# Performance work log

Hardware: AMD Instinct MI355X
Metric: run time of the kernel (lower is better)

## Reference

```python
import jax, jax.numpy as jnp
import numpy as np

NB = 4
QN = -(2 ** (NB - 1))   # -8
QP = 2 ** (NB - 1) - 1  # 7
EPS = 1e-5


def _grad_scale(x, g):
    # forward: x, backward: grad * g (LSQ gradient scaling)
    return x * g + jax.lax.stop_gradient(x - x * g)


def _round_pass(x):
    # round with straight-through estimator
    return x + jax.lax.stop_gradient(jnp.round(x) - x)


def _lsq(v, alpha, qn, qp):
    # LSQ fake quantize-dequantize with learnable step size alpha
    g = 1.0 / np.sqrt(v.size * qp)
    a = _grad_scale(alpha, g)
    return _round_pass(jnp.clip(v / a, qn, qp)) * a


def _bn(x, g, b, m, v):
    # eval-mode BatchNorm2d over channel dim of NCHW
    s = (g * jax.lax.rsqrt(v + EPS))[None, :, None, None]
    return (x - m[None, :, None, None]) * s + b[None, :, None, None]


def _conv(x, w, stride, pad, groups):
    return jax.lax.conv_general_dilated(
        x, w, (stride, stride), pad,
        dimension_numbers=('NCHW', 'OIHW', 'NCHW'),
        feature_group_count=groups)


def setup_inputs() -> dict:
    key = jax.random.key(0)
    ks = jax.random.split(key, 4)
    inp, oup, hid = 96, 96, 576
    B, H, W = 32, 28, 28
    d = {}
    d['x'] = jax.random.normal(ks[0], (B, inp, H, W), jnp.float32)
    d['w1'] = jax.random.normal(ks[1], (hid, inp, 1, 1), jnp.float32) * 0.1
    d['w2'] = jax.random.normal(ks[2], (hid, 1, 3, 3), jnp.float32) * 0.1
    d['w3'] = jax.random.normal(ks[3], (oup, hid, 1, 1), jnp.float32) * 0.1
    for i, c in zip((1, 2, 3), (hid, hid, oup)):
        d[f'aw{i}'] = jnp.full((1,), 0.05, jnp.float32)  # weight step size
        d[f'ax{i}'] = jnp.full((1,), 0.5, jnp.float32)   # activation step size
        d[f'g{i}'] = jnp.ones((c,), jnp.float32)
        d[f'b{i}'] = jnp.zeros((c,), jnp.float32)
        d[f'm{i}'] = jnp.zeros((c,), jnp.float32)
        d[f'v{i}'] = jnp.ones((c,), jnp.float32)
    return d


def reference(x, w1, w2, w3, aw1, ax1, g1, b1, m1, v1,
              aw2, ax2, g2, b2, m2, v2, aw3, ax3, g3, b3, m3, v3):
    hid = w1.shape[0]
    # 1x1 expand conv (LSQ on activation and weight)
    h = _conv(_lsq(x, ax1, QN, QP), _lsq(w1, aw1, QN, QP), 1, [(0, 0), (0, 0)], 1)
    h = jnp.clip(_bn(h, g1, b1, m1, v1), 0.0, 6.0)
    # 3x3 depthwise conv, stride 1
    h = _conv(_lsq(h, ax2, QN, QP), _lsq(w2, aw2, QN, QP), 1, [(1, 1), (1, 1)], hid)
    h = jnp.clip(_bn(h, g2, b2, m2, v2), 0.0, 6.0)
    # 1x1 project conv
    h = _conv(_lsq(h, ax3, QN, QP), _lsq(w3, aw3, QN, QP), 1, [(0, 0), (0, 0)], 1)
    h = _bn(h, g3, b3, m3, v3)
    # identity residual (stride==1 and inp==oup)
    return x + h
```

## Files before the change

### kernel.cpp

```cpp
#include <hip/hip_runtime.h>

#define EPSF 1e-5f
#define MAGICF 12582912.0f
#define MLO 0x4B3FFFF8
#define MHI 0x4B400007

typedef int    int4v   __attribute__((ext_vector_type(4)));
typedef float  float4v __attribute__((ext_vector_type(4)));

#define W1P_OFF  0
#define W3P_OFF  55296
#define W2T_OFF  110592
#define S1B1_OFF 119808
#define S2B2_OFF 124416
#define S3B3_OFF 129024

#define F1S 296
#define H2S 304

__device__ __forceinline__ float lsq_q(float v, float a) {
    float t = v / a;
    t = fminf(fmaxf(t, -8.0f), 7.0f);
    return rintf(t);
}

__device__ __forceinline__ long q8pack_w(const float* w, int base, const int* idx, float a) {
    unsigned long long v = 0;
    #pragma unroll
    for (int j = 0; j < 8; ++j) {
        int q = (int)lsq_q(w[base + idx[j]], a);
        v |= (unsigned long long)(q & 255) << (8 * j);
    }
    return (long)v;
}

__global__ __launch_bounds__(128)
void prep_w(const float* __restrict__ w1, const float* __restrict__ w2,
            const float* __restrict__ w3,
            const float* aw1, const float* ax1, const float* ax2,
            const float* aw2, const float* ax3, const float* aw3,
            const float* __restrict__ g1, const float* __restrict__ b1,
            const float* __restrict__ m1, const float* __restrict__ v1,
            const float* __restrict__ g2, const float* __restrict__ b2,
            const float* __restrict__ m2, const float* __restrict__ v2,
            const float* __restrict__ g3, const float* __restrict__ b3,
            const float* __restrict__ m3, const float* __restrict__ v3,
            long* __restrict__ w1p, long* __restrict__ w3p,
            int* __restrict__ w2t,
            float* __restrict__ s1b1, float* __restrict__ s2b2,
            float* __restrict__ s3b3) {
    int id = blockIdx.x * 128 + threadIdx.x;
    const int lin[8] = {0, 1, 2, 3, 4, 5, 6, 7};
    const int prm[8] = {0, 2, 4, 6, 1, 3, 5, 7};
    if (id < 6912) {
        int l = id & 63, t = id >> 6;
        int kc = t % 3, ct = t / 3;
        int co = ct * 16 + (l & 15);
        int ci0 = kc * 32 + (l >> 4) * 8;
        w1p[id] = q8pack_w(w1, co * 96 + ci0, lin, aw1[0]);
    } else if (id < 13824) {
        int i = id - 6912;
        int l = i & 63, t = i >> 6;
        int kc = t % 18, ct = t / 18;
        int co = ct * 16 + (l & 15);
        int ci0 = kc * 32 + (l >> 4) * 8;
        w3p[i] = q8pack_w(w3, co * 576 + ci0, prm, aw3[0]);
    } else if (id < 14400) {
        int ch = id - 13824;
        int q[9];
        #pragma unroll
        for (int tp = 0; tp < 9; ++tp)
            q[tp] = (int)lsq_q(w2[ch * 9 + tp], aw2[0]) & 255;
        w2t[ch * 4 + 0] = q[0] | (q[1] << 8) | (q[2] << 16) | (q[3] << 24);
        w2t[ch * 4 + 1] = q[4] | (q[5] << 8) | (q[6] << 16) | (q[7] << 24);
        w2t[ch * 4 + 2] = q[8];
        w2t[ch * 4 + 3] = 0;
    } else if (id < 14976) {
        int c = id - 14400;
        float s = g1[c] / sqrtf(v1[c] + EPSF);
        float A = aw1[0] * ax1[0];
        float inv = 1.0f / ax2[0];
        s1b1[c] = A * s * inv;
        s1b1[576 + c] = (b1[c] - m1[c] * s) * inv;
    } else if (id < 15552) {
        int c = id - 14976;
        float s = g2[c] / sqrtf(v2[c] + EPSF);
        float A = ax2[0] * aw2[0];
        float inv = 1.0f / ax3[0];
        s2b2[c] = A * s * inv;
        s2b2[576 + c] = (b2[c] - m2[c] * s) * inv;
    } else if (id < 15648) {
        int c = id - 15552;
        float s = g3[c] / sqrtf(v3[c] + EPSF);
        float A = ax3[0] * aw3[0];
        s3b3[c] = A * s;
        s3b3[96 + c] = b3[c] - m3[c] * s;
    }
}

__global__ __launch_bounds__(512, 4)
void fused_k(const float* __restrict__ x, const long* __restrict__ w1p,
             const int* __restrict__ w2tg, const long* __restrict__ w3p,
             const float* __restrict__ ax1,
             const float* __restrict__ s1b1g, const float* __restrict__ s2b2g,
             const float* __restrict__ s3b3g, float* __restrict__ out) {
    __shared__ __align__(16) char smem[74176];
    signed char* h1 = (signed char*)smem;
    float*       l1 = (float*)(smem + 35520);
    signed char* h2 = (signed char*)(smem + 40128);
    float*       l2 = (float*)(smem + 59584);
    float*       l3 = (float*)(smem + 64192);
    int4v*      l2t = (int4v*)(smem + 64960);
    long*    wstage = (long*)h2;
    long*       w3s = (long*)smem;

    const int tid = threadIdx.x;
    const int w = tid >> 6, l = tid & 63;
    const int quad = l >> 4, c16 = l & 15;
    const int qh = quad >> 1, ql = quad & 1;
    const int b = blockIdx.x;
    const int r0 = blockIdx.y * 2;
    const bool awork = (w < 7);

    {
        const int lp = w * 16 + c16;
        const int row = lp / 28, col = lp - (lp / 28) * 28;
        const int img_row = r0 - 1 + row;
        const bool valid = awork && ((unsigned)img_row < 28u);
        const int p = min(max(img_row, 0), 27) * 28 + col;
        const float inv1 = 1.0f / ax1[0];

        float xv[3][8];
        if (awork) {
            #pragma unroll
            for (int kc = 0; kc < 3; ++kc) {
                const float* xs = x + (b * 96 + kc * 32 + quad * 8) * 784 + p;
                #pragma unroll
                for (int j = 0; j < 8; ++j) xv[kc][j] = xs[j * 784];
            }
        }

        for (int i = tid; i < 35520 / 16; i += 512)
            ((int4v*)h1)[i] = (int4v){0, 0, 0, 0};
        if (tid < 288) {
            ((int4v*)l1)[tid] = ((const int4v*)s1b1g)[tid];
            ((int4v*)l2)[tid] = ((const int4v*)s2b2g)[tid];
        }
        if (tid < 48) ((int4v*)l3)[tid] = ((const int4v*)s3b3g)[tid];
        for (int i = tid; i < 576; i += 512) l2t[i] = ((const int4v*)w2tg)[i];
        for (int i = tid; i < 1152; i += 512) wstage[i] = w1p[i];
        __syncthreads();

        long bfr[3];
        if (awork) {
            #pragma unroll
            for (int kc = 0; kc < 3; ++kc) {
                unsigned long long v = 0;
                #pragma unroll
                for (int j = 0; j < 8; ++j) {
                    int qi = __float_as_int(fmaf(xv[kc][j], inv1, MAGICF));
                    qi = min(max(qi, MLO), MHI);
                    v |= (unsigned long long)(qi & 255) << (8 * j);
                }
                bfr[kc] = (long)v;
            }
        }
        const int pos_h = row * 30 + col + 1;

        for (int c = 0; c < 6; ++c) {
            if (!awork) {
                if (c < 5) {
                    const long* src = w1p + (c + 1) * 1152;
                    long stg[18];
                    #pragma unroll
                    for (int k = 0; k < 18; ++k) stg[k] = src[l + k * 64];
                    long* dst = wstage + ((c + 1) & 1) * 1152;
                    #pragma unroll
                    for (int k = 0; k < 18; ++k) dst[l + k * 64] = stg[k];
                }
            } else {
                const long* cur = wstage + (c & 1) * 1152;
                #pragma unroll 3
                for (int ctl = 0; ctl < 6; ++ctl) {
                    const int ct = c * 6 + ctl;
                    int4v acc; acc[0] = 0; acc[1] = 0; acc[2] = 0; acc[3] = 0;
                    #pragma unroll
                    for (int kc = 0; kc < 3; ++kc)
                        acc = __builtin_amdgcn_mfma_i32_16x16x32_i8(
                            cur[(ctl * 3 + kc) * 64 + l], bfr[kc], acc, 0, 0, 0);
                    const int co0 = ct * 16 + quad * 4;
                    float4v S = *(const float4v*)(l1 + co0);
                    float4v B = *(const float4v*)(l1 + 576 + co0);
                    int pk = 0;
                    #pragma unroll
                    for (int r2 = 0; r2 < 4; ++r2) {
                        float t = fmaf((float)acc[r2], S[r2], B[r2]);
                        t = __builtin_amdgcn_fmed3f(t, 0.0f, 7.0f);
                        pk |= (__float_as_int(t + MAGICF) & 15) << (4 * r2);
                    }
                    if (valid)
                        *(unsigned short*)(h1 + pos_h * F1S + (co0 >> 1))
                            = (unsigned short)pk;
                }
            }
            __syncthreads();
        }
    }

    {
        const bool vald = ((c16 >> 3) == ql);
        const int mh = c16 & 7;
        const int jj = (mh >> 1) | ((mh & 1) << 2);
        const unsigned shla = 8u * (jj & 3);
        const unsigned mlo = (jj < 4) ? 0xFFFFFFFFu : 0u;
        const unsigned mhi = ~mlo;
        const unsigned vm  = vald ? 0xFFu : 0u;
        const unsigned vm4 = (vald && qh == 0) ? 0xFFu : 0u;
        const unsigned sh0 = qh * 8u;
        const unsigned sh1 = 16u + qh * 8u;

        #pragma unroll 2
        for (int t = w; t < 144; t += 8) {
            const int pt = t / 36, ct = t - (t / 36) * 36;
            const int pos = pt * 16 + c16;
            const int posc = min(pos, 55);
            const int row_in = posc / 28, col = posc - (posc / 28) * 28;
            const int choff = ct * 8 + ql * 4;
            const int4v tw = l2t[ct * 16 + c16];
            int4v acc; acc[0] = 0; acc[1] = 0; acc[2] = 0; acc[3] = 0;
            #pragma unroll
            for (int kc = 0; kc < 5; ++kc) {
                unsigned bb;
                if      (kc == 0) bb = ((unsigned)tw[0] >> sh0) & vm;
                else if (kc == 1) bb = ((unsigned)tw[0] >> sh1) & vm;
                else if (kc == 2) bb = ((unsigned)tw[1] >> sh0) & vm;
                else if (kc == 3) bb = ((unsigned)tw[1] >> sh1) & vm;
                else              bb = ((unsigned)tw[2]) & vm4;
                const unsigned pl = bb << shla;
                const long afrag = (long)(((unsigned long long)(pl & mhi) << 32)
                                          | (pl & mlo));
                const int tap = min(kc * 2 + qh, 8);
                const int dh = tap / 3 - 1, dc = tap - (tap / 3) * 3 - 1;
                const int pos_h = (row_in + 1 + dh) * 30 + (col + 1 + dc);
                const unsigned v = *(const unsigned*)(h1 + pos_h * F1S + choff);
                const unsigned lo = v & 0x0F0F0F0Fu;
                const unsigned hi = (v >> 4) & 0x0F0F0F0Fu;
                acc = __builtin_amdgcn_mfma_i32_16x16x32_i8(
                    afrag, (long)(((unsigned long long)hi << 32) | lo), acc, 0, 0, 0);
            }
            if (pos < 56) {
                const int c0 = ct * 16 + quad * 4;
                float4v S = *(const float4v*)(l2 + c0);
                float4v B = *(const float4v*)(l2 + 576 + c0);
                int pk = 0;
                #pragma unroll
                for (int r2 = 0; r2 < 4; ++r2) {
                    float tt = fmaf((float)acc[r2], S[r2], B[r2]);
                    tt = __builtin_amdgcn_fmed3f(tt, 0.0f, 7.0f);
                    pk |= (__float_as_int(tt + MAGICF) & 15) << (4 * r2);
                }
                *(unsigned short*)(h2 + pos * H2S + (c0 >> 1)) = (unsigned short)pk;
            }
        }
    }

    {
        long stg[5];
        auto c3_issue = [&](int ck) {
            #pragma unroll
            for (int k = 0; k < 5; ++k) {
                const int e = tid + k * 512;
                if (e < 2304) {
                    const int ct2 = e / 384, rem = e - ct2 * 384;
                    stg[k] = w3p[ct2 * 1152 + ck * 384 + rem];
                }
            }
        };
        auto c3_write = [&](int buf) {
            #pragma unroll
            for (int k = 0; k < 5; ++k) {
                const int e = tid + k * 512;
                if (e < 2304) w3s[buf * 2304 + e] = stg[k];
            }
        };

        int4v accs[3];
        #pragma unroll
        for (int tt = 0; tt < 3; ++tt) {
            accs[tt][0] = 0; accs[tt][1] = 0; accs[tt][2] = 0; accs[tt][3] = 0;
        }
        auto c3_compute = [&](int ck, int buf) {
            #pragma unroll
            for (int tt = 0; tt < 3; ++tt) {
                const int t = w + tt * 8;
                const int nt = t / 6, ct = t - (t / 6) * 6;
                const signed char* arow = h2 + (nt * 16 + c16) * H2S + quad * 4;
                #pragma unroll
                for (int kcl = 0; kcl < 6; ++kcl) {
                    const int kc = ck * 6 + kcl;
                    const unsigned va = *(const unsigned*)(arow + kc * 16);
                    const unsigned lo = va & 0x0F0F0F0Fu;
                    const unsigned hi = (va >> 4) & 0x0F0F0F0Fu;
                    accs[tt] = __builtin_amdgcn_mfma_i32_16x16x32_i8(
                        (long)(((unsigned long long)hi << 32) | lo),
                        w3s[buf * 2304 + (ct * 6 + kcl) * 64 + l],
                        accs[tt], 0, 0, 0);
                }
            }
        };

        c3_issue(0);
        __syncthreads();
        c3_write(0);
        c3_issue(1);
        __syncthreads();
        c3_compute(0, 0);
        c3_write(1);
        c3_issue(2);
        __syncthreads();
        c3_compute(1, 1);
        c3_write(0);
        __syncthreads();
        c3_compute(2, 0);

        #pragma unroll
        for (int tt = 0; tt < 3; ++tt) {
            const int t = w + tt * 8;
            const int nt = t / 6, ct = t - (t / 6) * 6;
            const int nloc = nt * 16 + quad * 4;
            const int co = ct * 16 + c16;
            const int off = (b * 96 + co) * 784 + r0 * 28 + min(nloc, 52);
            if (nloc < 56) {
                const float4v xr = *(const float4v*)(x + off);
                const float S = l3[co], Bv = l3[96 + co];
                float4v o;
                #pragma unroll
                for (int r2 = 0; r2 < 4; ++r2)
                    o[r2] = fmaf((float)accs[tt][r2], S, Bv) + xr[r2];
                *(float4v*)(out + off) = o;
            }
        }
    }
}

extern "C" void kernel_launch(void* const* d_in, const int* in_sizes, int n_in,
                              void* d_out, int out_size, void* d_ws, size_t ws_size,
                              hipStream_t stream) {
    const float* x   = (const float*)d_in[0];
    const float* w1  = (const float*)d_in[1];
    const float* w2  = (const float*)d_in[2];
    const float* w3  = (const float*)d_in[3];
    const float* aw1 = (const float*)d_in[4];
    const float* ax1 = (const float*)d_in[5];
    const float* g1  = (const float*)d_in[6];
    const float* b1  = (const float*)d_in[7];
    const float* m1  = (const float*)d_in[8];
    const float* v1  = (const float*)d_in[9];
    const float* aw2 = (const float*)d_in[10];
    const float* ax2 = (const float*)d_in[11];
    const float* g2  = (const float*)d_in[12];
    const float* b2  = (const float*)d_in[13];
    const float* m2  = (const float*)d_in[14];
    const float* v2  = (const float*)d_in[15];
    const float* aw3 = (const float*)d_in[16];
    const float* ax3 = (const float*)d_in[17];
    const float* g3  = (const float*)d_in[18];
    const float* b3  = (const float*)d_in[19];
    const float* m3  = (const float*)d_in[20];
    const float* v3  = (const float*)d_in[21];

    char* ws = (char*)d_ws;
    long* w1p = (long*)(ws + W1P_OFF);
    long* w3p = (long*)(ws + W3P_OFF);
    int*  w2t = (int*)(ws + W2T_OFF);
    float* s1b1 = (float*)(ws + S1B1_OFF);
    float* s2b2 = (float*)(ws + S2B2_OFF);
    float* s3b3 = (float*)(ws + S3B3_OFF);

    float* out = (float*)d_out;

    prep_w<<<123, 128, 0, stream>>>(w1, w2, w3, aw1, ax1, ax2, aw2, ax3, aw3,
                                    g1, b1, m1, v1, g2, b2, m2, v2, g3, b3, m3, v3,
                                    w1p, w3p, w2t, s1b1, s2b2, s3b3);
    dim3 grid(32, 14);
    fused_k<<<grid, 512, 0, stream>>>(x, w1p, w2t, w3p, ax1, s1b1, s2b2, s3b3, out);
}
```

Before: 131.5 us.

## Interleave depthwise stage with expand-conv chunks and read w1 weights directly from global

After: 134.5 us. 2.2% more time.

```diff
diff --git a/kernel.cpp b/kernel.cpp
--- a/kernel.cpp
+++ b/kernel.cpp
@@ -111,7 +111,6 @@
     float*       l2 = (float*)(smem + 59584);
     float*       l3 = (float*)(smem + 64192);
     int4v*      l2t = (int4v*)(smem + 64960);
-    long*    wstage = (long*)h2;
     long*       w3s = (long*)smem;
 
     const int tid = threadIdx.x;
@@ -122,168 +121,155 @@
     const int r0 = blockIdx.y * 2;
     const bool awork = (w < 7);
 
-    {
-        const int lp = w * 16 + c16;
-        const int row = lp / 28, col = lp - (lp / 28) * 28;
-        const int img_row = r0 - 1 + row;
-        const bool valid = awork && ((unsigned)img_row < 28u);
-        const int p = min(max(img_row, 0), 27) * 28 + col;
-        const float inv1 = 1.0f / ax1[0];
-
-        float xv[3][8];
-        if (awork) {
+    const int lp = w * 16 + c16;
+    const int row = lp / 28, col = lp - (lp / 28) * 28;
+    const int img_row = r0 - 1 + row;
+    const bool valid = awork && ((unsigned)img_row < 28u);
+    const int p = min(max(img_row, 0), 27) * 28 + col;
+    const float inv1 = 1.0f / ax1[0];
+
+    float xv[3][8];
+    if (awork) {
+        #pragma unroll
+        for (int kc = 0; kc < 3; ++kc) {
+            const float* xs = x + (b * 96 + kc * 32 + quad * 8) * 784 + p;
             #pragma unroll
-            for (int kc = 0; kc < 3; ++kc) {
-                const float* xs = x + (b * 96 + kc * 32 + quad * 8) * 784 + p;
-                #pragma unroll
-                for (int j = 0; j < 8; ++j) xv[kc][j] = xs[j * 784];
-            }
-        }
-
-        for (int i = tid; i < 35520 / 16; i += 512)
-            ((int4v*)h1)[i] = (int4v){0, 0, 0, 0};
-        if (tid < 288) {
-            ((int4v*)l1)[tid] = ((const int4v*)s1b1g)[tid];
-            ((int4v*)l2)[tid] = ((const int4v*)s2b2g)[tid];
-        }
-        if (tid < 48) ((int4v*)l3)[tid] = ((const int4v*)s3b3g)[tid];
-        for (int i = tid; i < 576; i += 512) l2t[i] = ((const int4v*)w2tg)[i];
-        for (int i = tid; i < 1152; i += 512) wstage[i] = w1p[i];
-        __syncthreads();
-
-        long bfr[3];
-        if (awork) {
+            for (int j = 0; j < 8; ++j) xv[kc][j] = xs[j * 784];
+        }
+    }
+    for (int i = tid; i < 35520 / 16; i += 512)
+        ((int4v*)h1)[i] = (int4v){0, 0, 0, 0};
+    if (tid < 288) {
+        ((int4v*)l1)[tid] = ((const int4v*)s1b1g)[tid];
+        ((int4v*)l2)[tid] = ((const int4v*)s2b2g)[tid];
+    }
+    if (tid < 48) ((int4v*)l3)[tid] = ((const int4v*)s3b3g)[tid];
+    for (int i = tid; i < 576; i += 512) l2t[i] = ((const int4v*)w2tg)[i];
+    __syncthreads();
+
+    long bfr[3];
+    if (awork) {
+        #pragma unroll
+        for (int kc = 0; kc < 3; ++kc) {
+            unsigned long long v = 0;
             #pragma unroll
-            for (int kc = 0; kc < 3; ++kc) {
-                unsigned long long v = 0;
-                #pragma unroll
-                for (int j = 0; j < 8; ++j) {
-                    int qi = __float_as_int(fmaf(xv[kc][j], inv1, MAGICF));
-                    qi = min(max(qi, MLO), MHI);
-                    v |= (unsigned long long)(qi & 255) << (8 * j);
+            for (int j = 0; j < 8; ++j) {
+                int qi = __float_as_int(fmaf(xv[kc][j], inv1, MAGICF));
+                qi = min(max(qi, MLO), MHI);
+                v |= (unsigned long long)(qi & 255) << (8 * j);
+            }
+            bfr[kc] = (long)v;
+        }
+    }
+    const int pos_h = row * 30 + col + 1;
+
+    const bool vald = ((c16 >> 3) == ql);
+    const int mh = c16 & 7;
+    const int jj = (mh >> 1) | ((mh & 1) << 2);
+    const unsigned shla = 8u * (jj & 3);
+    const unsigned mloM = (jj < 4) ? 0xFFFFFFFFu : 0u;
+    const unsigned mhiM = ~mloM;
+    const unsigned vm  = vald ? 0xFFu : 0u;
+    const unsigned vm4 = (vald && qh == 0) ? 0xFFu : 0u;
+    const unsigned sh0 = qh * 8u;
+    const unsigned sh1 = 16u + qh * 8u;
+
+    long stg[5];
+    auto c3_issue = [&](int ck) {
+        #pragma unroll
+        for (int k = 0; k < 5; ++k) {
+            const int e = tid + k * 512;
+            if (e < 2304) {
+                const int ct2 = e / 384, rem = e - ct2 * 384;
+                stg[k] = w3p[ct2 * 1152 + ck * 384 + rem];
+            }
+        }
+    };
+    auto c3_write = [&](int buf) {
+        #pragma unroll
+        for (int k = 0; k < 5; ++k) {
+            const int e = tid + k * 512;
+            if (e < 2304) w3s[buf * 2304 + e] = stg[k];
+        }
+    };
+
+    for (int c = 0; c < 7; ++c) {
+        if (c < 6 && awork) {
+            #pragma unroll 2
+            for (int ctl = 0; ctl < 6; ++ctl) {
+                const int ct = c * 6 + ctl;
+                int4v acc; acc[0] = 0; acc[1] = 0; acc[2] = 0; acc[3] = 0;
+                #pragma unroll
+                for (int kc = 0; kc < 3; ++kc)
+                    acc = __builtin_amdgcn_mfma_i32_16x16x32_i8(
+                        w1p[(ct * 3 + kc) * 64 + l], bfr[kc], acc, 0, 0, 0);
+                const int co0 = ct * 16 + quad * 4;
+                float4v S = *(const float4v*)(l1 + co0);
+                float4v B = *(const float4v*)(l1 + 576 + co0);
+                int pk = 0;
+                #pragma unroll
+                for (int r2 = 0; r2 < 4; ++r2) {
+                    float t = fmaf((float)acc[r2], S[r2], B[r2]);
+                    t = __builtin_amdgcn_fmed3f(t, 0.0f, 7.0f);
+                    pk |= (__float_as_int(t + MAGICF) & 15) << (4 * r2);
                 }
-                bfr[kc] = (long)v;
-            }
-        }
-        const int pos_h = row * 30 + col + 1;
-
-        for (int c = 0; c < 6; ++c) {
-            if (!awork) {
-                if (c < 5) {
-                    const long* src = w1p + (c + 1) * 1152;
-                    long stg[18];
-                    #pragma unroll
-                    for (int k = 0; k < 18; ++k) stg[k] = src[l + k * 64];
-                    long* dst = wstage + ((c + 1) & 1) * 1152;
-                    #pragma unroll
-                    for (int k = 0; k < 18; ++k) dst[l + k * 64] = stg[k];
+                if (valid)
+                    *(unsigned short*)(h1 + pos_h * F1S + (co0 >> 1))
+                        = (unsigned short)pk;
+            }
+        }
+        if (c >= 1) {
+            #pragma unroll
+            for (int i = 0; i < 3; ++i) {
+                const int t = w + i * 8;
+                const int pt = t / 6, ctl = t - (t / 6) * 6;
+                const int ct = (c - 1) * 6 + ctl;
+                const int pos = pt * 16 + c16;
+                const int posc = min(pos, 55);
+                const int row_in = posc / 28, bcol = posc - (posc / 28) * 28;
+                const int choff = ct * 8 + ql * 4;
+                const int4v tw = l2t[ct * 16 + c16];
+                int4v acc; acc[0] = 0; acc[1] = 0; acc[2] = 0; acc[3] = 0;
+                #pragma unroll
+                for (int kc = 0; kc < 5; ++kc) {
+                    unsigned bb;
+                    if      (kc == 0) bb = ((unsigned)tw[0] >> sh0) & vm;
+                    else if (kc == 1) bb = ((unsigned)tw[0] >> sh1) & vm;
+                    else if (kc == 2) bb = ((unsigned)tw[1] >> sh0) & vm;
+                    else if (kc == 3) bb = ((unsigned)tw[1] >> sh1) & vm;
+                    else              bb = ((unsigned)tw[2]) & vm4;
+                    const unsigned pl = bb << shla;
+                    const long afrag = (long)(((unsigned long long)(pl & mhiM) << 32)
+                                              | (pl & mloM));
+                    const int tap = min(kc * 2 + qh, 8);
+                    const int dh = tap / 3 - 1, dc = tap - (tap / 3) * 3 - 1;
+                    const int ph = (row_in + 1 + dh) * 30 + (bcol + 1 + dc);
+                    const unsigned v = *(const unsigned*)(h1 + ph * F1S + choff);
+                    const unsigned lo = v & 0x0F0F0F0Fu;
+                    const unsigned hi = (v >> 4) & 0x0F0F0F0Fu;
+                    acc = __builtin_amdgcn_mfma_i32_16x16x32_i8(
+                        afrag, (long)(((unsigned long long)hi << 32) | lo), acc, 0, 0, 0);
                 }
-            } else {
-                const long* cur = wstage + (c & 1) * 1152;
-                #pragma unroll 3
-                for (int ctl = 0; ctl < 6; ++ctl) {
-                    const int ct = c * 6 + ctl;
-                    int4v acc; acc[0] = 0; acc[1] = 0; acc[2] = 0; acc[3] = 0;
-                    #pragma unroll
-                    for (int kc = 0; kc < 3; ++kc)
-                        acc = __builtin_amdgcn_mfma_i32_16x16x32_i8(
-                            cur[(ctl * 3 + kc) * 64 + l], bfr[kc], acc, 0, 0, 0);
-                    const int co0 = ct * 16 + quad * 4;
-                    float4v S = *(const float4v*)(l1 + co0);
-                    float4v B = *(const float4v*)(l1 + 576 + co0);
+                if (pos < 56) {
+                    const int c0 = ct * 16 + quad * 4;
+                    float4v S = *(const float4v*)(l2 + c0);
+                    float4v B = *(const float4v*)(l2 + 576 + c0);
                     int pk = 0;
                     #pragma unroll
                     for (int r2 = 0; r2 < 4; ++r2) {
-                        float t = fmaf((float)acc[r2], S[r2], B[r2]);
-                        t = __builtin_amdgcn_fmed3f(t, 0.0f, 7.0f);
-                        pk |= (__float_as_int(t + MAGICF) & 15) << (4 * r2);
+                        float tt = fmaf((float)acc[r2], S[r2], B[r2]);
+                        tt = __builtin_amdgcn_fmed3f(tt, 0.0f, 7.0f);
+                        pk |= (__float_as_int(tt + MAGICF) & 15) << (4 * r2);
                     }
-                    if (valid)
-                        *(unsigned short*)(h1 + pos_h * F1S + (co0 >> 1))
-                            = (unsigned short)pk;
+                    *(unsigned short*)(h2 + pos * H2S + (c0 >> 1)) = (unsigned short)pk;
                 }
             }
-            __syncthreads();
-        }
+        }
+        if (c == 6) c3_issue(0);
+        __syncthreads();
     }
 
     {
-        const bool vald = ((c16 >> 3) == ql);
-        const int mh = c16 & 7;
-        const int jj = (mh >> 1) | ((mh & 1) << 2);
-        const unsigned shla = 8u * (jj & 3);
-        const unsigned mlo = (jj < 4) ? 0xFFFFFFFFu : 0u;
-        const unsigned mhi = ~mlo;
-        const unsigned vm  = vald ? 0xFFu : 0u;
-        const unsigned vm4 = (vald && qh == 0) ? 0xFFu : 0u;
-        const unsigned sh0 = qh * 8u;
-        const unsigned sh1 = 16u + qh * 8u;
-
-        #pragma unroll 2
-        for (int t = w; t < 144; t += 8) {
-            const int pt = t / 36, ct = t - (t / 36) * 36;
-            const int pos = pt * 16 + c16;
-            const int posc = min(pos, 55);
-            const int row_in = posc / 28, col = posc - (posc / 28) * 28;
-            const int choff = ct * 8 + ql * 4;
-            const int4v tw = l2t[ct * 16 + c16];
-            int4v acc; acc[0] = 0; acc[1] = 0; acc[2] = 0; acc[3] = 0;
-            #pragma unroll
-            for (int kc = 0; kc < 5; ++kc) {
-                unsigned bb;
-                if      (kc == 0) bb = ((unsigned)tw[0] >> sh0) & vm;
-                else if (kc == 1) bb = ((unsigned)tw[0] >> sh1) & vm;
-                else if (kc == 2) bb = ((unsigned)tw[1] >> sh0) & vm;
-                else if (kc == 3) bb = ((unsigned)tw[1] >> sh1) & vm;
-                else              bb = ((unsigned)tw[2]) & vm4;
-                const unsigned pl = bb << shla;
-                const long afrag = (long)(((unsigned long long)(pl & mhi) << 32)
-                                          | (pl & mlo));
-                const int tap = min(kc * 2 + qh, 8);
-                const int dh = tap / 3 - 1, dc = tap - (tap / 3) * 3 - 1;
-                const int pos_h = (row_in + 1 + dh) * 30 + (col + 1 + dc);
-                const unsigned v = *(const unsigned*)(h1 + pos_h * F1S + choff);
-                const unsigned lo = v & 0x0F0F0F0Fu;
-                const unsigned hi = (v >> 4) & 0x0F0F0F0Fu;
-                acc = __builtin_amdgcn_mfma_i32_16x16x32_i8(
-                    afrag, (long)(((unsigned long long)hi << 32) | lo), acc, 0, 0, 0);
-            }
-            if (pos < 56) {
-                const int c0 = ct * 16 + quad * 4;
-                float4v S = *(const float4v*)(l2 + c0);
-                float4v B = *(const float4v*)(l2 + 576 + c0);
-                int pk = 0;
-                #pragma unroll
-                for (int r2 = 0; r2 < 4; ++r2) {
-                    float tt = fmaf((float)acc[r2], S[r2], B[r2]);
-                    tt = __builtin_amdgcn_fmed3f(tt, 0.0f, 7.0f);
-                    pk |= (__float_as_int(tt + MAGICF) & 15) << (4 * r2);
-                }
-                *(unsigned short*)(h2 + pos * H2S + (c0 >> 1)) = (unsigned short)pk;
-            }
-        }
-    }
-
-    {
-        long stg[5];
-        auto c3_issue = [&](int ck) {
-            #pragma unroll
-            for (int k = 0; k < 5; ++k) {
-                const int e = tid + k * 512;
-                if (e < 2304) {
-                    const int ct2 = e / 384, rem = e - ct2 * 384;
-                    stg[k] = w3p[ct2 * 1152 + ck * 384 + rem];
-                }
-            }
-        };
-        auto c3_write = [&](int buf) {
-            #pragma unroll
-            for (int k = 0; k < 5; ++k) {
-                const int e = tid + k * 512;
-                if (e < 2304) w3s[buf * 2304 + e] = stg[k];
-            }
-        };
-
         int4v accs[3];
         #pragma unroll
         for (int tt = 0; tt < 3; ++tt) {
@@ -309,8 +295,6 @@
             }
         };
 
-        c3_issue(0);
-        __syncthreads();
         c3_write(0);
         c3_issue(1);
         __syncthreads();
```
